# Kernel optimization log

Hardware: AMD Instinct MI355X
Metric: run time of the kernel (lower is better)

## Reference

```python
import jax, jax.numpy as jnp
import numpy as np
import math

B, S, D, H, DK, FF, L = 4, 1024, 512, 8, 64, 2048, 4
IN, NS, SD, TOPK = 768, 4, 64, 2


def _ln(x, g, b, eps=1e-5):
    mu = jnp.mean(x, -1, keepdims=True)
    var = jnp.mean((x - mu) ** 2, -1, keepdims=True)
    return (x - mu) / jnp.sqrt(var + eps) * g + b


def _pos_emb(s, d):
    pos = jnp.arange(s, dtype=jnp.float32)[:, None]
    div = jnp.exp(jnp.arange(0, d, 2, dtype=jnp.float32) * (-math.log(10000.0) / d))
    pe = jnp.zeros((s, d), jnp.float32)
    pe = pe.at[:, 0::2].set(jnp.sin(pos * div))
    pe = pe.at[:, 1::2].set(jnp.cos(pos * div))
    return pe


def setup_inputs() -> dict:
    key = jax.random.key(0)
    ks = iter(jax.random.split(key, 40))
    r = lambda *sh: jax.random.normal(next(ks), sh, jnp.float32)
    p = lambda *sh: jax.random.normal(next(ks), sh, jnp.float32) * 0.02
    inp = {
        'q_raw_seq': r(B, S, NS, IN),
        'm_seq': r(B, S, SD),
        'qa_embed': r(B, S, D),
        # MoE expert FFNs: Linear(IN,IN) -> ReLU -> Linear(IN,D)
        'exp_w1': p(NS, IN, IN), 'exp_b1': jnp.zeros((NS, IN)),
        'exp_w2': p(NS, IN, D), 'exp_b2': jnp.zeros((NS, D)),
        # router input adapter Linear(NS*IN, D)
        'adapt_w': p(NS * IN, D), 'adapt_b': jnp.zeros((D,)),
        'gate_w': p(D + SD, NS), 'gate_b': jnp.zeros((NS,)),
        'moe_ln_g': jnp.ones((D,)), 'moe_ln_b': jnp.zeros((D,)),
        # transformer blocks (kq_same=1 -> k_linear shared for q and k)
        'kw': p(L, D, D), 'kb': jnp.zeros((L, D)),
        'vw': p(L, D, D), 'vb': jnp.zeros((L, D)),
        'ow': p(L, D, D), 'ob': jnp.zeros((L, D)),
        'ln1_g': jnp.ones((L, D)), 'ln1_b': jnp.zeros((L, D)),
        'ff_w1': p(L, D, FF), 'ff_b1': jnp.zeros((L, FF)),
        'ff_w2': p(L, FF, D), 'ff_b2': jnp.zeros((L, D)),
        'ln2_g': jnp.ones((L, D)), 'ln2_b': jnp.zeros((L, D)),
    }
    return inp


def _forward(q_raw_seq, m_seq, qa_embed, exp_w1, exp_b1, exp_w2, exp_b2,
             adapt_w, adapt_b, gate_w, gate_b, moe_ln_g, moe_ln_b,
             kw, kb, vw, vb, ow, ob, ln1_g, ln1_b,
             ff_w1, ff_b1, ff_w2, ff_b2, ln2_g, ln2_b):
    # ---- PolyaParallelMoE (eval: no noise/dropout), has_stages=True ----
    h1 = jax.nn.relu(jnp.einsum('bske,kef->bskf', q_raw_seq, exp_w1) + exp_b1[None, None])
    experts = jnp.einsum('bskf,kfm->bskm', h1, exp_w2) + exp_b2[None, None]  # [B,S,4,D]
    q_flat = q_raw_seq.reshape(q_raw_seq.shape[0], q_raw_seq.shape[1], NS * IN)
    summary = jax.nn.relu(q_flat @ adapt_w + adapt_b)
    logits = jnp.concatenate([summary, m_seq], -1) @ gate_w + gate_b  # [B,S,4]
    top_vals, _ = jax.lax.top_k(logits, TOPK)
    thresh = top_vals[..., -1:]
    masked = jnp.where(logits >= thresh, logits, -jnp.inf)  # scatter top-k, -inf elsewhere
    gate_weights = jax.nn.softmax(masked, -1)
    combined = jnp.einsum('bskm,bsk->bsm', experts, gate_weights)
    q_embed = _ln(combined, moe_ln_g, moe_ln_b)

    # ---- Architecture: positional add + causal transformer blocks ----
    pe = _pos_emb(S, D)
    x = q_embed + pe
    y = qa_embed + pe
    allow = jnp.tril(jnp.ones((S, S), bool), -1)  # strict lower: np.triu(k=0)==0
    scale = 1.0 / math.sqrt(DK)
    for i in range(L):
        kh = (x @ kw[i] + kb[i]).reshape(B, S, H, DK).transpose(0, 2, 1, 3)
        vh = (y @ vw[i] + vb[i]).reshape(B, S, H, DK).transpose(0, 2, 1, 3)
        # kq_same: q = k_linear(query), query==key==x -> qh == kh
        scores = jnp.einsum('bhid,bhjd->bhij', kh, kh) * scale
        scores = jnp.where(allow, scores, -1e32)
        attn = jax.nn.softmax(scores, -1)
        attn = attn.at[:, :, 0, :].set(0.0)  # zero_pad first query row
        ctx = jnp.einsum('bhij,bhjd->bhid', attn, vh).transpose(0, 2, 1, 3).reshape(B, S, D)
        x = _ln(x + (ctx @ ow[i] + ob[i]), ln1_g[i], ln1_b[i])
        ffn = jax.nn.relu(x @ ff_w1[i] + ff_b1[i]) @ ff_w2[i] + ff_b2[i]
        x = _ln(x + ffn, ln2_g[i], ln2_b[i])
        y = x  # after first block, value stream follows torch loop (values=y fixed)
        y = qa_embed + pe  # values stay qa stream per Architecture.forward
    return x


def reference(q_raw_seq, m_seq, qa_embed, exp_w1, exp_b1, exp_w2, exp_b2,
              adapt_w, adapt_b, gate_w, gate_b, moe_ln_g, moe_ln_b,
              kw, kb, vw, vb, ow, ob, ln1_g, ln1_b,
              ff_w1, ff_b1, ff_w2, ff_b2, ln2_g, ln2_b):
    # NOTE: in Architecture.forward, each block is called with query=x, key=x, values=y
    # where y = qa_embed + pe stays fixed across blocks.
    def fwd(*a):
        return _forward(*a)
    return fwd(q_raw_seq, m_seq, qa_embed, exp_w1, exp_b1, exp_w2, exp_b2,
               adapt_w, adapt_b, gate_w, gate_b, moe_ln_g, moe_ln_b,
               kw, kb, vw, vb, ow, ob, ln1_g, ln1_b,
               ff_w1, ff_b1, ff_w2, ff_b2, ln2_g, ln2_b)
```

## Files before the change

kernel.cpp:

```cpp
#include <hip/hip_runtime.h>
#include <hip/hip_bf16.h>

typedef unsigned short u16;
typedef __attribute__((ext_vector_type(8))) short short8;
typedef __attribute__((ext_vector_type(4))) float floatx4;

__device__ __forceinline__ float bf2f(u16 u) {
    unsigned x = (unsigned)u << 16;
    return __uint_as_float(x);
}
__device__ __forceinline__ u16 f2bf(float f) {
    unsigned x = __float_as_uint(f);
    unsigned r = (x + 0x7fffu + ((x >> 16) & 1u)) >> 16;
    return (u16)r;
}

__device__ __forceinline__ float wave_sum(float v) {
    #pragma unroll
    for (int off = 32; off; off >>= 1) v += __shfl_xor(v, off);
    return v;
}

__device__ __forceinline__ void async16(const u16* g, const u16* lds) {
    __builtin_amdgcn_global_load_lds(
        (const __attribute__((address_space(1))) void*)g,
        (__attribute__((address_space(3))) void*)lds, 16, 0, 0);
}

__device__ __forceinline__ void hilo8(const float* p, u16* hi, u16* lo) {
    float4 a = *(const float4*)p, b = *(const float4*)(p + 4);
    float v[8] = {a.x, a.y, a.z, a.w, b.x, b.y, b.z, b.w};
    #pragma unroll
    for (int i = 0; i < 8; ++i) {
        u16 h = f2bf(v[i]);
        hi[i] = h;
        lo[i] = f2bf(v[i] - bf2f(h));
    }
}

__global__ __launch_bounds__(256) void hilo_conv_kernel(
    const float* __restrict__ in, u16* __restrict__ hi, u16* __restrict__ lo)
{
    const size_t i = ((size_t)blockIdx.x * 256 + threadIdx.x) * 8;
    u16 h[8], l[8];
    hilo8(in + i, h, l);
    *(uint4*)&hi[i] = *(const uint4*)h;
    *(uint4*)&lo[i] = *(const uint4*)l;
}

__device__ __forceinline__ void gemm_body(
    const u16* __restrict__ A, int lda,
    const u16* __restrict__ Bt, int ldb,
    const float* __restrict__ bias,
    float* __restrict__ Cf, u16* __restrict__ Cb, int ldc,
    int K, int act, int transC, int m0, int n0)
{
    __shared__ __align__(16) u16 Asm[2][8192];
    __shared__ __align__(16) u16 Bsm[2][8192];

    const int tid = threadIdx.x;
    const int lane = tid & 63;
    const int wave = tid >> 6;
    const int wm = (wave >> 1) * 64, wn = (wave & 1) * 64;

    const int r0 = tid >> 2;
    const int kc = (tid & 3) * 8;
    const int kq = (lane >> 4) * 8;
    const int fm = lane & 15;

    const floatx4 zz = {0.f, 0.f, 0.f, 0.f};
    floatx4 acc[4][4];
    #pragma unroll
    for (int mt = 0; mt < 4; ++mt)
        #pragma unroll
        for (int nt = 0; nt < 4; ++nt) acc[mt][nt] = zz;

    auto stage = [&](int kt, int b) {
        #pragma unroll
        for (int h = 0; h < 2; ++h) {
            async16(&A[(size_t)(m0 + r0) * lda + kt + h * 32 + kc],      &Asm[b][h * 4096 + wave * 512]);
            async16(&A[(size_t)(m0 + r0 + 64) * lda + kt + h * 32 + kc], &Asm[b][h * 4096 + 2048 + wave * 512]);
            async16(&Bt[(size_t)(n0 + r0) * ldb + kt + h * 32 + kc],      &Bsm[b][h * 4096 + wave * 512]);
            async16(&Bt[(size_t)(n0 + r0 + 64) * ldb + kt + h * 32 + kc], &Bsm[b][h * 4096 + 2048 + wave * 512]);
        }
    };

    stage(0, 0);
    __syncthreads();

    for (int kt = 0; kt < K; kt += 64) {
        const int cur = (kt >> 6) & 1;
        const bool more = (kt + 64 < K);
        if (more) stage(kt + 64, cur ^ 1);

        #pragma unroll
        for (int h = 0; h < 2; ++h) {
            short8 af[4], bfr[4];
            #pragma unroll
            for (int mt = 0; mt < 4; ++mt)
                af[mt] = *(const short8*)&Asm[cur][h * 4096 + (wm + mt * 16 + fm) * 32 + kq];
            #pragma unroll
            for (int nt = 0; nt < 4; ++nt)
                bfr[nt] = *(const short8*)&Bsm[cur][h * 4096 + (wn + nt * 16 + fm) * 32 + kq];

            #pragma unroll
            for (int mt = 0; mt < 4; ++mt)
                #pragma unroll
                for (int nt = 0; nt < 4; ++nt)
                    acc[mt][nt] = __builtin_amdgcn_mfma_f32_16x16x32_bf16(
                        af[mt], bfr[nt], acc[mt][nt], 0, 0, 0);
        }
        if (more) __syncthreads();
    }

    const int cr = (lane >> 4) * 4;
    #pragma unroll
    for (int mt = 0; mt < 4; ++mt) {
        #pragma unroll
        for (int nt = 0; nt < 4; ++nt) {
            const int col = n0 + wn + nt * 16 + fm;
            const float bz = bias ? bias[col] : 0.f;
            #pragma unroll
            for (int r = 0; r < 4; ++r) {
                const int row = m0 + wm + mt * 16 + cr + r;
                float v = acc[mt][nt][r] + bz;
                if (act) v = fmaxf(v, 0.f);
                if (Cf) Cf[(size_t)row * ldc + col] = v;
                if (Cb) {
                    if (transC)
                        Cb[(((size_t)(row >> 10) * 512 + col) << 10) + (row & 1023)] = f2bf(v);
                    else
                        Cb[(size_t)row * ldc + col] = f2bf(v);
                }
            }
        }
    }
}

template <typename TA>
__global__ __launch_bounds__(256) void gemm_bf16(
    const TA* __restrict__ A, int lda, long strideAz,
    const u16* __restrict__ Bt, int ldb, long strideBz,
    const float* __restrict__ bias, int strideBiasZ,
    float* __restrict__ Cf, u16* __restrict__ Cb, int ldc, long strideCz,
    int K, int act, int transC, int NT)
{
    const int wg   = blockIdx.x;
    const int xcd  = wg & 7;
    const int slot = wg >> 3;
    const int nt   = slot % NT;
    const int pg   = slot / NT;
    const int panel = xcd + 8 * pg;
    const int my = panel & 31, mz = panel >> 5;

    A  += (size_t)mz * strideAz;
    Bt += (size_t)mz * strideBz;
    const float* bz = bias ? bias + (size_t)mz * strideBiasZ : nullptr;
    if (Cf) Cf += (size_t)mz * strideCz;
    if (Cb) Cb += (size_t)mz * strideCz;
    gemm_body(A, lda, Bt, ldb, bz, Cf, Cb, ldc, K, act, transC, my * 128, nt * 128);
}

__global__ __launch_bounds__(256) void gemm_kv(
    const u16* __restrict__ xb, const u16* __restrict__ yb,
    const u16* __restrict__ kwt, const u16* __restrict__ vwt,
    const float* __restrict__ kb, const float* __restrict__ vb,
    u16* __restrict__ khb, u16* __restrict__ vhT)
{
    const int wg   = blockIdx.x;
    const int xcd  = wg & 7;
    const int slot = wg >> 3;
    const int nt   = slot & 3;
    const int pg   = slot >> 2;
    const int panel = xcd + 8 * pg;
    const int my = panel & 31, mz = panel >> 5;

    if (mz == 0)
        gemm_body(xb, 512, kwt, 512, kb, nullptr, khb, 512, 512, 0, 0, my * 128, nt * 128);
    else
        gemm_body(yb, 512, vwt, 512, vb, nullptr, vhT, 512, 512, 0, 1, my * 128, nt * 128);
}

__global__ __launch_bounds__(256) void gemm_f32split(
    const u16* __restrict__ Ah, const u16* __restrict__ Al, int lda,
    const u16* __restrict__ Bh, const u16* __restrict__ Bl, int ldb,
    float* __restrict__ Cf, int ldc, long strideCz,
    int kz)
{
    __shared__ __align__(16) u16 Ahs[2][4096];
    __shared__ __align__(16) u16 Als[2][4096];
    __shared__ __align__(16) u16 Bhs[2][4096];
    __shared__ __align__(16) u16 Bls[2][4096];

    const int wg   = blockIdx.x;
    const int xcd  = wg & 7;
    const int slot = wg >> 3;
    const int nt4  = slot & 3;
    const int g    = xcd + 8 * (slot >> 2);
    const int my   = g & 31, mz = g >> 5;

    const int tid = threadIdx.x;
    const int lane = tid & 63;
    const int wave = tid >> 6;
    const int m0 = my * 128, n0 = nt4 * 128;
    const int wm = (wave >> 1) * 64, wn = (wave & 1) * 64;
    const int k0 = mz * kz;
    Cf += (size_t)mz * strideCz;

    const int r0 = tid >> 2;
    const int kc = (tid & 3) * 8;
    const int kq = (lane >> 4) * 8;
    const int fm = lane & 15;

    const floatx4 zz = {0.f, 0.f, 0.f, 0.f};
    floatx4 acc[4][4];
    #pragma unroll
    for (int mt = 0; mt < 4; ++mt)
        #pragma unroll
        for (int nt = 0; nt < 4; ++nt) acc[mt][nt] = zz;

    auto stage = [&](int kt, int b) {
        const size_t ka = (size_t)(m0 + r0) * lda + k0 + kt + kc;
        const size_t kb = (size_t)(n0 + r0) * ldb + k0 + kt + kc;
        async16(&Ah[ka],                    &Ahs[b][wave * 512]);
        async16(&Ah[ka + (size_t)64 * lda], &Ahs[b][2048 + wave * 512]);
        async16(&Al[ka],                    &Als[b][wave * 512]);
        async16(&Al[ka + (size_t)64 * lda], &Als[b][2048 + wave * 512]);
        async16(&Bh[kb],                    &Bhs[b][wave * 512]);
        async16(&Bh[kb + (size_t)64 * ldb], &Bhs[b][2048 + wave * 512]);
        async16(&Bl[kb],                    &Bls[b][wave * 512]);
        async16(&Bl[kb + (size_t)64 * ldb], &Bls[b][2048 + wave * 512]);
    };

    stage(0, 0);
    __syncthreads();

    for (int kt = 0; kt < kz; kt += 32) {
        const int cur = (kt >> 5) & 1;
        const bool more = (kt + 32 < kz);
        if (more) stage(kt + 32, cur ^ 1);

        short8 ah[4], al[4], bh[4], bl[4];
        #pragma unroll
        for (int mt = 0; mt < 4; ++mt) {
            ah[mt] = *(const short8*)&Ahs[cur][(wm + mt * 16 + fm) * 32 + kq];
            al[mt] = *(const short8*)&Als[cur][(wm + mt * 16 + fm) * 32 + kq];
        }
        #pragma unroll
        for (int nt = 0; nt < 4; ++nt) {
            bh[nt] = *(const short8*)&Bhs[cur][(wn + nt * 16 + fm) * 32 + kq];
            bl[nt] = *(const short8*)&Bls[cur][(wn + nt * 16 + fm) * 32 + kq];
        }

        #pragma unroll
        for (int mt = 0; mt < 4; ++mt)
            #pragma unroll
            for (int nt = 0; nt < 4; ++nt) {
                acc[mt][nt] = __builtin_amdgcn_mfma_f32_16x16x32_bf16(
                    ah[mt], bh[nt], acc[mt][nt], 0, 0, 0);
                acc[mt][nt] = __builtin_amdgcn_mfma_f32_16x16x32_bf16(
                    al[mt], bh[nt], acc[mt][nt], 0, 0, 0);
                acc[mt][nt] = __builtin_amdgcn_mfma_f32_16x16x32_bf16(
                    ah[mt], bl[nt], acc[mt][nt], 0, 0, 0);
            }
        if (more) __syncthreads();
    }

    const int cr = (lane >> 4) * 4;
    #pragma unroll
    for (int mt = 0; mt < 4; ++mt) {
        #pragma unroll
        for (int nt = 0; nt < 4; ++nt) {
            const int col = n0 + wn + nt * 16 + fm;
            #pragma unroll
            for (int r = 0; r < 4; ++r) {
                const int row = m0 + wm + mt * 16 + cr + r;
                Cf[(size_t)row * ldc + col] = acc[mt][nt][r];
            }
        }
    }
}

__global__ __launch_bounds__(64) void gate_fused_kernel(
    const float* __restrict__ ps, const float* __restrict__ adapt_b,
    const float* __restrict__ m_seq,
    const float* __restrict__ gw, const float* __restrict__ gb,
    float* __restrict__ gates)
{
    const int r = blockIdx.x, t = threadIdx.x;
    float p0 = 0.f, p1 = 0.f, p2 = 0.f, p3 = 0.f;
    const float* pr = ps + (size_t)r * 512;
    for (int j = t; j < 512; j += 64) {
        float v = pr[j] + pr[j + 2097152] + pr[j + 4194304] + pr[j + 6291456] + adapt_b[j];
        float s = fmaxf(v, 0.f);
        const float* g = gw + (size_t)j * 4;
        p0 += s * g[0]; p1 += s * g[1]; p2 += s * g[2]; p3 += s * g[3];
    }
    {
        float m = m_seq[(size_t)r * 64 + t];
        const float* g = gw + (size_t)(512 + t) * 4;
        p0 += m * g[0]; p1 += m * g[1]; p2 += m * g[2]; p3 += m * g[3];
    }
    p0 = wave_sum(p0); p1 = wave_sum(p1); p2 = wave_sum(p2); p3 = wave_sum(p3);
    if (t == 0) {
        float lg[4] = { p0 + gb[0], p1 + gb[1], p2 + gb[2], p3 + gb[3] };
        float m1 = -INFINITY, m2 = -INFINITY;
        #pragma unroll
        for (int k = 0; k < 4; ++k) {
            float v = lg[k];
            if (v > m1) { m2 = m1; m1 = v; }
            else if (v > m2) { m2 = v; }
        }
        float wv[4], s = 0.f;
        #pragma unroll
        for (int k = 0; k < 4; ++k) {
            wv[k] = (lg[k] >= m2) ? __expf(lg[k] - m1) : 0.f;
            s += wv[k];
        }
        float inv = 1.f / s;
        #pragma unroll
        for (int k = 0; k < 4; ++k) gates[(size_t)r * 4 + k] = wv[k] * inv;
    }
}

__global__ __launch_bounds__(256) void tconv_kernel(
    const float* __restrict__ in, u16* __restrict__ out, int K, int N)
{
    __shared__ float t[32][33];
    const int n0 = blockIdx.x * 32, k0 = blockIdx.y * 32;
    const size_t bo = (size_t)blockIdx.z * K * N;
    const int tx = threadIdx.x & 31, ty = threadIdx.x >> 5;
    const float* src = in + bo;
    u16* dst = out + bo;
    #pragma unroll
    for (int r = ty; r < 32; r += 8) t[r][tx] = src[(size_t)(k0 + r) * N + n0 + tx];
    __syncthreads();
    #pragma unroll
    for (int r = ty; r < 32; r += 8) dst[(size_t)(n0 + r) * K + k0 + tx] = f2bf(t[tx][r]);
}

__global__ __launch_bounds__(256) void tconv3_kernel(
    const float* __restrict__ kw, const float* __restrict__ vw, const float* __restrict__ ow,
    u16* __restrict__ kwt, u16* __restrict__ vwt, u16* __restrict__ owt)
{
    __shared__ float t[32][33];
    const int z = blockIdx.z;
    const int sel = z >> 2, li = z & 3;
    const float* in = (sel == 0) ? kw : (sel == 1) ? vw : ow;
    u16* outp = (sel == 0) ? kwt : (sel == 1) ? vwt : owt;
    const size_t bo = (size_t)li * 262144;
    const int n0 = blockIdx.x * 32, k0 = blockIdx.y * 32;
    const int tx = threadIdx.x & 31, ty = threadIdx.x >> 5;
    const float* src = in + bo;
    u16* dst = outp + bo;
    #pragma unroll
    for (int r = ty; r < 32; r += 8) t[r][tx] = src[(size_t)(k0 + r) * 512 + n0 + tx];
    __syncthreads();
    #pragma unroll
    for (int r = ty; r < 32; r += 8) dst[(size_t)(n0 + r) * 512 + k0 + tx] = f2bf(t[tx][r]);
}

__global__ __launch_bounds__(256) void tconv_hilo_kernel(
    const float* __restrict__ in, u16* __restrict__ outh, u16* __restrict__ outl,
    int K, int N)
{
    __shared__ float t[32][33];
    const int n0 = blockIdx.x * 32, k0 = blockIdx.y * 32;
    const int tx = threadIdx.x & 31, ty = threadIdx.x >> 5;
    #pragma unroll
    for (int r = ty; r < 32; r += 8) t[r][tx] = in[(size_t)(k0 + r) * N + n0 + tx];
    __syncthreads();
    #pragma unroll
    for (int r = ty; r < 32; r += 8) {
        float v = t[tx][r];
        u16 h = f2bf(v);
        outh[(size_t)(n0 + r) * K + k0 + tx] = h;
        outl[(size_t)(n0 + r) * K + k0 + tx] = f2bf(v - bf2f(h));
    }
}

__global__ void pe_kernel(float* __restrict__ pe)
{
    int idx = blockIdx.x * 256 + threadIdx.x;
    int s = idx >> 9, d = idx & 511;
    float div = expf((float)(d & ~1) * (-9.210340371976184f / 512.0f));
    float ang = (float)s * div;
    pe[idx] = (d & 1) ? cosf(ang) : sinf(ang);
}

__global__ __launch_bounds__(64) void moe_ln_kernel(
    const u16* __restrict__ experts, const float* __restrict__ gates,
    const float* __restrict__ g, const float* __restrict__ bb,
    const float* __restrict__ pe, const float* __restrict__ qa,
    float* __restrict__ x, u16* __restrict__ xb, u16* __restrict__ yb)
{
    const int r = blockIdx.x, t = threadIdx.x;
    const u16* e = experts + (size_t)r * 2048;
    const float g0 = gates[r * 4 + 0], g1 = gates[r * 4 + 1];
    const float g2 = gates[r * 4 + 2], g3 = gates[r * 4 + 3];
    float v[8];
    #pragma unroll
    for (int it = 0; it < 8; ++it) {
        int d = t + it * 64;
        v[it] = g0 * bf2f(e[d]) + g1 * bf2f(e[512 + d])
              + g2 * bf2f(e[1024 + d]) + g3 * bf2f(e[1536 + d]);
    }
    float s = 0.f;
    #pragma unroll
    for (int it = 0; it < 8; ++it) s += v[it];
    s = wave_sum(s);
    const float mu = s * (1.f / 512.f);
    float q = 0.f;
    #pragma unroll
    for (int it = 0; it < 8; ++it) { float dd = v[it] - mu; q += dd * dd; }
    q = wave_sum(q);
    const float rstd = rsqrtf(q * (1.f / 512.f) + 1e-5f);
    const float* per = pe + (size_t)(r & 1023) * 512;
    #pragma unroll
    for (int it = 0; it < 8; ++it) {
        int d = t + it * 64;
        float pv = per[d];
        float o = (v[it] - mu) * rstd * g[d] + bb[d] + pv;
        x[(size_t)r * 512 + d] = o;
        xb[(size_t)r * 512 + d] = f2bf(o);
        yb[(size_t)r * 512 + d] = f2bf(qa[(size_t)r * 512 + d] + pv);
    }
}

__global__ __launch_bounds__(64) void add_ln_kernel(
    float* __restrict__ x, u16* __restrict__ xb,
    const float* __restrict__ t0, const float* __restrict__ t1,
    const float* __restrict__ bias,
    const float* __restrict__ g, const float* __restrict__ bb,
    float* __restrict__ out2)
{
    const int r = blockIdx.x, t = threadIdx.x;
    float* xr = x + (size_t)r * 512;
    float v[8];
    #pragma unroll
    for (int it = 0; it < 8; ++it) {
        int d = t + it * 64;
        float tv = t0[(size_t)r * 512 + d];
        if (t1) tv += t1[(size_t)r * 512 + d];
        if (bias) tv += bias[d];
        v[it] = xr[d] + tv;
    }
    float s = 0.f;
    #pragma unroll
    for (int it = 0; it < 8; ++it) s += v[it];
    s = wave_sum(s);
    const float mu = s * (1.f / 512.f);
    float q = 0.f;
    #pragma unroll
    for (int it = 0; it < 8; ++it) { float dd = v[it] - mu; q += dd * dd; }
    q = wave_sum(q);
    const float rstd = rsqrtf(q * (1.f / 512.f) + 1e-5f);
    #pragma unroll
    for (int it = 0; it < 8; ++it) {
        int d = t + it * 64;
        float o = (v[it] - mu) * rstd * g[d] + bb[d];
        xr[d] = o;
        xb[(size_t)r * 512 + d] = f2bf(o);
        if (out2) out2[(size_t)r * 512 + d] = o;
    }
}

__global__ __launch_bounds__(256) void attn_kernel(
    const u16* __restrict__ kh, const u16* __restrict__ vhT,
    u16* __restrict__ ctx)
{
    __shared__ __align__(16) u16 Qs[64 * 64];
    __shared__ __align__(16) u16 Ks[2][64 * 64];
    __shared__ __align__(16) u16 Vt[2][64 * 72];
    __shared__ __align__(16) u16 Ps[64 * 72];

    const int tid = threadIdx.x;
    const int lane = tid & 63, wave = tid >> 6;
    const int quad = lane >> 4, fm = lane & 15;
    const int b = blockIdx.x, h = blockIdx.y;
    const int bz = blockIdx.z;
    const int it = (bz < 8) ? bz : (23 - bz);

    const u16* khb = kh + ((size_t)b * 1024) * 512 + h * 64;
    const u16* vtb = vhT + ((size_t)(b * 512 + h * 64)) * 1024;

    const int lj = tid >> 2;
    const int lc = tid & 3;

    {
        const u16* src = khb + (size_t)(it * 64 + lj) * 512 + lc * 16;
        *(uint4*)&Qs[lj * 64 + lc * 16]     = *(const uint4*)src;
        *(uint4*)&Qs[lj * 64 + lc * 16 + 8] = *(const uint4*)(src + 8);
    }

    {
        const u16* ksrc = khb + (size_t)(lj) * 512 + lc * 16;
        *(uint4*)&Ks[0][lj * 64 + lc * 16]     = *(const uint4*)ksrc;
        *(uint4*)&Ks[0][lj * 64 + lc * 16 + 8] = *(const uint4*)(ksrc + 8);
        const u16* vsrc = vtb + (size_t)lj * 1024 + lc * 16;
        *(uint4*)&Vt[0][lj * 72 + lc * 16]     = *(const uint4*)vsrc;
        *(uint4*)&Vt[0][lj * 72 + lc * 16 + 8] = *(const uint4*)(vsrc + 8);
    }

    const floatx4 zz = {0.f, 0.f, 0.f, 0.f};
    floatx4 o_acc[4];
    #pragma unroll
    for (int nt = 0; nt < 4; ++nt) o_acc[nt] = zz;
    float m_run[4] = { -INFINITY, -INFINITY, -INFINITY, -INFINITY };
    float l_run[4] = {};

    __syncthreads();

    for (int jt = 0; jt <= it; ++jt) {
        const int cur = jt & 1;
        const bool pf = (jt < it);

        uint4 kr0, kr1, vr0, vr1;
        if (pf) {
            const u16* ksrc = khb + (size_t)((jt + 1) * 64 + lj) * 512 + lc * 16;
            kr0 = *(const uint4*)ksrc;
            kr1 = *(const uint4*)(ksrc + 8);
            const u16* vsrc = vtb + (size_t)lj * 1024 + (jt + 1) * 64 + lc * 16;
            vr0 = *(const uint4*)vsrc;
            vr1 = *(const uint4*)(vsrc + 8);
        }

        floatx4 s_acc[4];
        #pragma unroll
        for (int nt = 0; nt < 4; ++nt) s_acc[nt] = zz;
        #pragma unroll
        for (int ks = 0; ks < 2; ++ks) {
            short8 af = *(const short8*)&Qs[(wave * 16 + fm) * 64 + ks * 32 + quad * 8];
            #pragma unroll
            for (int nt = 0; nt < 4; ++nt) {
                short8 bf = *(const short8*)&Ks[cur][(nt * 16 + fm) * 64 + ks * 32 + quad * 8];
                s_acc[nt] = __builtin_amdgcn_mfma_f32_16x16x32_bf16(af, bf, s_acc[nt], 0, 0, 0);
            }
        }

        const bool diag = (jt == it);
        #pragma unroll
        for (int r = 0; r < 4; ++r) {
            const int rowi = wave * 16 + quad * 4 + r;
            float sv[4];
            #pragma unroll
            for (int nt = 0; nt < 4; ++nt) {
                float s = s_acc[nt][r] * 0.125f;
                if (diag && (nt * 16 + fm) >= rowi) s = -INFINITY;
                sv[nt] = s;
            }
            float mx = fmaxf(fmaxf(sv[0], sv[1]), fmaxf(sv[2], sv[3]));
            #pragma unroll
            for (int off = 1; off < 16; off <<= 1) mx = fmaxf(mx, __shfl_xor(mx, off));
            const float mn = fmaxf(m_run[r], mx);
            const float mfix = (mn == -INFINITY) ? 0.f : mn;
            const float alpha = (m_run[r] == -INFINITY) ? 0.f : __expf(m_run[r] - mn);
            m_run[r] = mn;
            float rs = 0.f;
            #pragma unroll
            for (int nt = 0; nt < 4; ++nt) {
                float p = __expf(sv[nt] - mfix);
                Ps[rowi * 72 + nt * 16 + fm] = f2bf(p);
                rs += p;
            }
            #pragma unroll
            for (int off = 1; off < 16; off <<= 1) rs += __shfl_xor(rs, off);
            l_run[r] = l_run[r] * alpha + rs;
            #pragma unroll
            for (int nt = 0; nt < 4; ++nt) o_acc[nt][r] *= alpha;
        }

        #pragma unroll
        for (int ks = 0; ks < 2; ++ks) {
            short8 af = *(const short8*)&Ps[(wave * 16 + fm) * 72 + ks * 32 + quad * 8];
            #pragma unroll
            for (int nt = 0; nt < 4; ++nt) {
                short8 bf = *(const short8*)&Vt[cur][(nt * 16 + fm) * 72 + ks * 32 + quad * 8];
                o_acc[nt] = __builtin_amdgcn_mfma_f32_16x16x32_bf16(af, bf, o_acc[nt], 0, 0, 0);
            }
        }

        if (pf) {
            *(uint4*)&Ks[cur ^ 1][lj * 64 + lc * 16]     = kr0;
            *(uint4*)&Ks[cur ^ 1][lj * 64 + lc * 16 + 8] = kr1;
            *(uint4*)&Vt[cur ^ 1][lj * 72 + lc * 16]     = vr0;
            *(uint4*)&Vt[cur ^ 1][lj * 72 + lc * 16 + 8] = vr1;
            __syncthreads();
        }
    }

    u16* cb = ctx + ((size_t)b * 1024 + (size_t)it * 64 + wave * 16) * 512 + h * 64;
    #pragma unroll
    for (int r = 0; r < 4; ++r) {
        const int row = quad * 4 + r;
        const float inv = (l_run[r] > 0.f) ? 1.f / l_run[r] : 0.f;
        #pragma unroll
        for (int nt = 0; nt < 4; ++nt)
            cb[(size_t)row * 512 + nt * 16 + fm] = f2bf(o_acc[nt][r] * inv);
    }
}

extern "C" void kernel_launch(void* const* d_in, const int* in_sizes, int n_in,
                              void* d_out, int out_size, void* d_ws, size_t ws_size,
                              hipStream_t stream)
{
    const float* q_raw   = (const float*)d_in[0];
    const float* m_seq   = (const float*)d_in[1];
    const float* qa      = (const float*)d_in[2];
    const float* exp_w1  = (const float*)d_in[3];
    const float* exp_b1  = (const float*)d_in[4];
    const float* exp_w2  = (const float*)d_in[5];
    const float* exp_b2  = (const float*)d_in[6];
    const float* adapt_w = (const float*)d_in[7];
    const float* adapt_b = (const float*)d_in[8];
    const float* gate_w  = (const float*)d_in[9];
    const float* gate_b  = (const float*)d_in[10];
    const float* moe_g   = (const float*)d_in[11];
    const float* moe_b   = (const float*)d_in[12];
    const float* kw      = (const float*)d_in[13];
    const float* kb      = (const float*)d_in[14];
    const float* vw      = (const float*)d_in[15];
    const float* vb      = (const float*)d_in[16];
    const float* ow      = (const float*)d_in[17];
    const float* ob      = (const float*)d_in[18];
    const float* ln1g    = (const float*)d_in[19];
    const float* ln1b    = (const float*)d_in[20];
    const float* fw1     = (const float*)d_in[21];
    const float* fb1     = (const float*)d_in[22];
    const float* fw2     = (const float*)d_in[23];
    const float* fb2     = (const float*)d_in[24];
    const float* ln2g    = (const float*)d_in[25];
    const float* ln2b    = (const float*)d_in[26];
    float* out = (float*)d_out;

    const size_t NEED = 125829120ull;
    if (ws_size < NEED) return;

    char* base = (char*)d_ws;
    float* x  = (float*)(base + 0);
    u16*  xb  = (u16*)(base + 8388608);
    u16*  yb  = (u16*)(base + 12582912);
    char* G = base + 16777216;
    u16*   w1t     = (u16*)(G + 0);
    u16*   w2t     = (u16*)(G + 4718592);
    float* psum    = (float*)(G + 7864320);
    u16*   h1b4    = (u16*)(G + 7864320);
    u16*   expb    = (u16*)(G + 33030144);
    float* pe      = (float*)(G + 49807360);
    float* gates   = (float*)(G + 51904512);
    u16*   adwh    = (u16*)(G + 52428800);
    u16*   adwl    = (u16*)(G + 55574528);
    u16*   qhi     = (u16*)(G + 58720256);
    u16*   qlo     = (u16*)(G + 83886080);
    u16*   kwt  = (u16*)(G + 0);
    u16*   vwt  = (u16*)(G + 2097152);
    u16*   owt  = (u16*)(G + 4194304);
    u16*   fw1t = (u16*)(G + 6291456);
    u16*   fw2t = (u16*)(G + 14680064);
    u16*   khb  = (u16*)(G + 23068672);
    u16*   vhT  = (u16*)(G + 27262976);
    u16*   ctxb = (u16*)(G + 31457280);
    float* p    = (float*)(G + 35651584);
    u16*   ffhb = (u16*)(G + 44040192);
    float* ps0  = (float*)(G + 23068672);

    pe_kernel<<<2048, 256, 0, stream>>>(pe);
    hilo_conv_kernel<<<6144, 256, 0, stream>>>(q_raw, qhi, qlo);
    tconv_kernel<<<dim3(24, 24, 4), 256, 0, stream>>>(exp_w1, w1t, 768, 768);
    tconv_kernel<<<dim3(16, 24, 4), 256, 0, stream>>>(exp_w2, w2t, 768, 512);
    tconv_hilo_kernel<<<dim3(16, 96), 256, 0, stream>>>(adapt_w, adwh, adwl, 3072, 512);

    gemm_f32split<<<512, 256, 0, stream>>>(
        qhi, qlo, 3072, adwh, adwl, 3072, psum, 512, 2097152L, 768);
    gate_fused_kernel<<<4096, 64, 0, stream>>>(
        psum, adapt_b, m_seq, gate_w, gate_b, gates);

    gemm_bf16<u16><<<768, 256, 0, stream>>>(
        qhi, 3072, 768L, w1t, 768, 589824L, exp_b1, 768,
        nullptr, h1b4, 768, 3145728L, 768, 1, 0, 6);
    gemm_bf16<u16><<<512, 256, 0, stream>>>(
        h1b4, 768, 3145728L, w2t, 768, 393216L, exp_b2, 512,
        nullptr, expb, 2048, 512L, 768, 0, 0, 4);
    moe_ln_kernel<<<4096, 64, 0, stream>>>(expb, gates, moe_g, moe_b, pe, qa, x, xb, yb);

    tconv3_kernel<<<dim3(16, 16, 12), 256, 0, stream>>>(kw, vw, ow, kwt, vwt, owt);
    tconv_kernel<<<dim3(64, 16, 4), 256, 0, stream>>>(fw1, fw1t, 512, 2048);
    tconv_kernel<<<dim3(16, 64, 4), 256, 0, stream>>>(fw2, fw2t, 2048, 512);

    for (int i = 0; i < 4; ++i) {
        gemm_kv<<<256, 256, 0, stream>>>(
            xb, yb, kwt + (size_t)i * 262144, vwt + (size_t)i * 262144,
            kb + i * 512, vb + i * 512, khb, vhT);
        attn_kernel<<<dim3(4, 8, 16), 256, 0, stream>>>(khb, vhT, ctxb);
        gemm_bf16<u16><<<128, 256, 0, stream>>>(
            ctxb, 512, 0L, owt + (size_t)i * 262144, 512, 0L, ob + i * 512, 0,
            p, nullptr, 512, 0L, 512, 0, 0, 4);
        add_ln_kernel<<<4096, 64, 0, stream>>>(
            x, xb, p, nullptr, nullptr, ln1g + i * 512, ln1b + i * 512, nullptr);
        gemm_bf16<u16><<<512, 256, 0, stream>>>(
            xb, 512, 0L, fw1t + (size_t)i * 1048576, 512, 0L, fb1 + i * 2048, 0,
            nullptr, ffhb, 2048, 0L, 512, 1, 0, 16);
        gemm_bf16<u16><<<256, 256, 0, stream>>>(
            ffhb, 2048, 1024L, fw2t + (size_t)i * 1048576, 2048, 1024L, nullptr, 0,
            ps0, nullptr, 512, 2097152L, 1024, 0, 0, 4);
        add_ln_kernel<<<4096, 64, 0, stream>>>(
            x, xb, ps0, ps0 + 2097152, fb2 + i * 512,
            ln2g + i * 512, ln2b + i * 512, (i == 3) ? out : nullptr);
    }
}
```

Before: 905.7 us.

## Use partial vmcnt waits and raw barriers to overlap async loads in GEMMs

```diff
diff --git a/kernel.cpp b/kernel.cpp
--- a/kernel.cpp
+++ b/kernel.cpp
@@ -55,8 +55,8 @@
     float* __restrict__ Cf, u16* __restrict__ Cb, int ldc,
     int K, int act, int transC, int m0, int n0)
 {
-    __shared__ __align__(16) u16 Asm[2][8192];
-    __shared__ __align__(16) u16 Bsm[2][8192];
+    __shared__ __align__(16) u16 Asm[2][4096];
+    __shared__ __align__(16) u16 Bsm[2][4096];
 
     const int tid = threadIdx.x;
     const int lane = tid & 63;
@@ -76,41 +76,45 @@
         for (int nt = 0; nt < 4; ++nt) acc[mt][nt] = zz;
 
     auto stage = [&](int kt, int b) {
-        #pragma unroll
-        for (int h = 0; h < 2; ++h) {
-            async16(&A[(size_t)(m0 + r0) * lda + kt + h * 32 + kc],      &Asm[b][h * 4096 + wave * 512]);
-            async16(&A[(size_t)(m0 + r0 + 64) * lda + kt + h * 32 + kc], &Asm[b][h * 4096 + 2048 + wave * 512]);
-            async16(&Bt[(size_t)(n0 + r0) * ldb + kt + h * 32 + kc],      &Bsm[b][h * 4096 + wave * 512]);
-            async16(&Bt[(size_t)(n0 + r0 + 64) * ldb + kt + h * 32 + kc], &Bsm[b][h * 4096 + 2048 + wave * 512]);
-        }
+        async16(&A[(size_t)(m0 + r0) * lda + kt + kc],      &Asm[b][wave * 512]);
+        async16(&A[(size_t)(m0 + r0 + 64) * lda + kt + kc], &Asm[b][2048 + wave * 512]);
+        async16(&Bt[(size_t)(n0 + r0) * ldb + kt + kc],      &Bsm[b][wave * 512]);
+        async16(&Bt[(size_t)(n0 + r0 + 64) * ldb + kt + kc], &Bsm[b][2048 + wave * 512]);
     };
 
     stage(0, 0);
-    __syncthreads();
-
-    for (int kt = 0; kt < K; kt += 64) {
-        const int cur = (kt >> 6) & 1;
-        const bool more = (kt + 64 < K);
-        if (more) stage(kt + 64, cur ^ 1);
-
-        #pragma unroll
-        for (int h = 0; h < 2; ++h) {
-            short8 af[4], bfr[4];
-            #pragma unroll
-            for (int mt = 0; mt < 4; ++mt)
-                af[mt] = *(const short8*)&Asm[cur][h * 4096 + (wm + mt * 16 + fm) * 32 + kq];
+
+    for (int kt = 0; kt < K; kt += 32) {
+        const int cur = (kt >> 5) & 1;
+        const bool more = (kt + 32 < K);
+        if (more) {
+            stage(kt + 32, cur ^ 1);
+            asm volatile("s_waitcnt vmcnt(4)" ::: "memory");
+        } else {
+            asm volatile("s_waitcnt vmcnt(0)" ::: "memory");
+        }
+        __builtin_amdgcn_s_barrier();
+        __builtin_amdgcn_sched_barrier(0);
+
+        short8 af[4], bfr[4];
+        #pragma unroll
+        for (int mt = 0; mt < 4; ++mt)
+            af[mt] = *(const short8*)&Asm[cur][(wm + mt * 16 + fm) * 32 + kq];
+        #pragma unroll
+        for (int nt = 0; nt < 4; ++nt)
+            bfr[nt] = *(const short8*)&Bsm[cur][(wn + nt * 16 + fm) * 32 + kq];
+
+        #pragma unroll
+        for (int mt = 0; mt < 4; ++mt)
             #pragma unroll
             for (int nt = 0; nt < 4; ++nt)
-                bfr[nt] = *(const short8*)&Bsm[cur][h * 4096 + (wn + nt * 16 + fm) * 32 + kq];
-
-            #pragma unroll
-            for (int mt = 0; mt < 4; ++mt)
-                #pragma unroll
-                for (int nt = 0; nt < 4; ++nt)
-                    acc[mt][nt] = __builtin_amdgcn_mfma_f32_16x16x32_bf16(
-                        af[mt], bfr[nt], acc[mt][nt], 0, 0, 0);
-        }
-        if (more) __syncthreads();
+                acc[mt][nt] = __builtin_amdgcn_mfma_f32_16x16x32_bf16(
+                    af[mt], bfr[nt], acc[mt][nt], 0, 0, 0);
+
+        if (more) {
+            __builtin_amdgcn_s_barrier();
+            __builtin_amdgcn_sched_barrier(0);
+        }
     }
 
     const int cr = (lane >> 4) * 4;
@@ -233,12 +237,18 @@
     };
 
     stage(0, 0);
-    __syncthreads();
 
     for (int kt = 0; kt < kz; kt += 32) {
         const int cur = (kt >> 5) & 1;
         const bool more = (kt + 32 < kz);
-        if (more) stage(kt + 32, cur ^ 1);
+        if (more) {
+            stage(kt + 32, cur ^ 1);
+            asm volatile("s_waitcnt vmcnt(8)" ::: "memory");
+        } else {
+            asm volatile("s_waitcnt vmcnt(0)" ::: "memory");
+        }
+        __builtin_amdgcn_s_barrier();
+        __builtin_amdgcn_sched_barrier(0);
 
         short8 ah[4], al[4], bh[4], bl[4];
         #pragma unroll
@@ -263,7 +273,11 @@
                 acc[mt][nt] = __builtin_amdgcn_mfma_f32_16x16x32_bf16(
                     ah[mt], bl[nt], acc[mt][nt], 0, 0, 0);
             }
-        if (more) __syncthreads();
+
+        if (more) {
+            __builtin_amdgcn_s_barrier();
+            __builtin_amdgcn_sched_barrier(0);
+        }
     }
 
     const int cr = (lane >> 4) * 4;
```

Measured after the change: 988.1 us. 1.09x slower.
